# Optimization experiments

Hardware: AMD Instinct MI355X
Metric: run time of the kernel (lower is better)

## Reference

```python
import jax, jax.numpy as jnp
import numpy as np

EPS = 1e-6
LN3 = 1.0986122886681098  # ternary_softmax uses base-3 exponentials: 3**x / sum(3**x)
ROPE_BASE = 10000.0


def exact_rmsnorm(x, g):
    # ExactRMSNorm: x / sqrt(mean(x^2) + eps) * g
    ms = jnp.mean(jnp.square(x), axis=-1, keepdims=True)
    return x * jax.lax.rsqrt(ms + EPS) * g


def ternary_rope(t):
    # Rotary embedding whose cos/sin tables are quantized to {-1, 0, +1}
    # (round() of cos/sin in [-1,1] yields exactly the ternary set).
    S, D = t.shape[-2], t.shape[-1]
    half = D // 2
    inv_freq = 1.0 / (ROPE_BASE ** (jnp.arange(half, dtype=jnp.float32) / half))
    ang = jnp.arange(S, dtype=jnp.float32)[:, None] * inv_freq[None, :]  # [S, half]
    cos = jnp.round(jnp.cos(ang))
    sin = jnp.round(jnp.sin(ang))
    cos = jnp.concatenate([cos, cos], axis=-1)  # [S, D]
    sin = jnp.concatenate([sin, sin], axis=-1)
    rot = jnp.concatenate([-t[..., half:], t[..., :half]], axis=-1)
    return t * cos + rot * sin


def ternary_softmax(x, axis=-1):
    # softmax in base 3: 3**x / sum(3**x) == softmax(x * ln 3)
    return jax.nn.softmax(x * LN3, axis=axis)


def setup_inputs() -> dict:
    key = jax.random.key(0)
    ks = jax.random.split(key, 6)
    B, S, D = 4, 4096, 1024
    x = jax.random.normal(ks[0], (B, S, D), dtype=jnp.float32)
    g_norm = jnp.ones((D,), dtype=jnp.float32)
    w_qkv = jax.random.normal(ks[1], (D, 3 * D), dtype=jnp.float32) * 0.02
    b_qkv = jnp.zeros((3 * D,), dtype=jnp.float32)
    w_proj = jax.random.normal(ks[2], (D, D), dtype=jnp.float32) * 0.02
    b_proj = jnp.zeros((D,), dtype=jnp.float32)
    return {"x": x, "g_norm": g_norm, "w_qkv": w_qkv, "b_qkv": b_qkv,
            "w_proj": w_proj, "b_proj": b_proj}


def reference(x, g_norm, w_qkv, b_qkv, w_proj, b_proj):
    D = x.shape[-1]
    scale = 1.0 / jnp.sqrt(jnp.float32(D))
    residual = x
    h = exact_rmsnorm(x, g_norm)
    qkv = h @ w_qkv + b_qkv  # [B, S, 3D]
    q, k, v = jnp.split(qkv, 3, axis=-1)
    q = ternary_rope(q)
    k = ternary_rope(k)
    scores = jnp.einsum("bsd,btd->bst", q, k) * scale  # [B, S, S]
    attn = ternary_softmax(scores, axis=-1)
    o = jnp.einsum("bst,btd->bsd", attn, v)
    return o @ w_proj + b_proj + residual
```

## Files before the change

kernel.cpp:

```cpp
#include <hip/hip_runtime.h>
#include <hip/hip_fp8.h>
#include <stdint.h>

#define DEVI __device__ __forceinline__

typedef unsigned short u16;
typedef uint8_t u8;
typedef __attribute__((ext_vector_type(8))) __bf16 bf16x8;
typedef __attribute__((ext_vector_type(4))) float f32x4;
typedef __attribute__((ext_vector_type(4))) int i32x4;
typedef __attribute__((ext_vector_type(8))) int i32x8;

DEVI float b2f(u16 u) { union { unsigned int i; float f; } v; v.i = ((unsigned int)u) << 16; return v.f; }
DEVI u16 f2b(float f) {
  union { float f; unsigned int i; } v; v.f = f;
  unsigned int r = v.i + 0x7fffu + ((v.i >> 16) & 1u);
  return (u16)(r >> 16);
}
DEVI u8 f2f8(float f) { __hip_fp8_e4m3 t(f); return t.__x; }

DEVI void gld_lds16(const void* g, void* l) {
  __builtin_amdgcn_global_load_lds((const __attribute__((address_space(1))) unsigned int*)g,
                                   (__attribute__((address_space(3))) unsigned int*)l, 16, 0, 0);
}

DEVI i32x8 ld32(const u8* p0, const u8* p1) {
  i32x4 lo = *(const i32x4*)p0;
  i32x4 hi = *(const i32x4*)p1;
  return __builtin_shufflevector(lo, hi, 0, 1, 2, 3, 4, 5, 6, 7);
}


__global__ __launch_bounds__(256) void k_rmsnorm(const float* __restrict__ x,
                                                 const float* __restrict__ g,
                                                 u8* __restrict__ h) {
  const int row = blockIdx.x;
  const int t = threadIdx.x;
  const float4 v = ((const float4*)(x + (size_t)row * 1024))[t];
  float ss = v.x * v.x + v.y * v.y + v.z * v.z + v.w * v.w;
  for (int off = 32; off > 0; off >>= 1) ss += __shfl_down(ss, off);
  __shared__ float red[4];
  if ((t & 63) == 0) red[t >> 6] = ss;
  __syncthreads();
  const float tot = red[0] + red[1] + red[2] + red[3];
  const float sc = rsqrtf(tot * (1.0f / 1024.0f) + 1e-6f);
  const float4 gv = ((const float4*)g)[t];
  uchar4 o;
  o.x = f2f8(v.x * sc * gv.x); o.y = f2f8(v.y * sc * gv.y);
  o.z = f2f8(v.z * sc * gv.z); o.w = f2f8(v.w * sc * gv.w);
  *(uchar4*)(h + (size_t)row * 1024 + t * 4) = o;
}

__global__ __launch_bounds__(256) void k_transpose_cast(const float* __restrict__ src,
                                                        int rows, int cols,
                                                        u16* __restrict__ dst) {
  __shared__ float tile[32][33];
  const int c0 = blockIdx.x * 32, r0 = blockIdx.y * 32;
  const int tx = threadIdx.x, ty = threadIdx.y;
  for (int i = 0; i < 32; i += 8)
    tile[ty + i][tx] = src[(size_t)(r0 + ty + i) * cols + c0 + tx];
  __syncthreads();
  for (int i = 0; i < 32; i += 8)
    dst[(size_t)(c0 + ty + i) * rows + r0 + tx] = f2b(tile[tx][ty + i]);
}

__global__ __launch_bounds__(256) void k_transpose_cast_f8(const float* __restrict__ src,
                                                           int rows, int cols,
                                                           u8* __restrict__ dst) {
  __shared__ float tile[32][33];
  const int c0 = blockIdx.x * 32, r0 = blockIdx.y * 32;
  const int tx = threadIdx.x, ty = threadIdx.y;
  for (int i = 0; i < 32; i += 8)
    tile[ty + i][tx] = src[(size_t)(r0 + ty + i) * cols + c0 + tx];
  __syncthreads();
  for (int i = 0; i < 32; i += 8)
    dst[(size_t)(c0 + ty + i) * rows + r0 + tx] = f2f8(tile[tx][ty + i] * 32.0f);
}

__global__ __launch_bounds__(256) void k_rope_cast(const u16* __restrict__ q16, const u16* __restrict__ k16,
                                                   u8* __restrict__ q8, u8* __restrict__ k8) {
  const int row = blockIdx.x;
  const int pos = row & 4095;
  const int t = threadIdx.x;
  const int j0 = t * 2;
  float c[2], s[2];
#pragma unroll
  for (int u = 0; u < 2; u++) {
    const float e = (float)(j0 + u) * (1.0f / 512.0f);
    const float invf = exp2f(-13.287712379549449f * e);
    const float ang = (float)pos * invf;
    c[u] = rintf(cosf(ang));
    s[u] = rintf(sinf(ang));
  }
  const u16* qr = q16 + (size_t)row * 1024;
  const u16* kr = k16 + (size_t)row * 1024;
  u8* qo = q8 + (size_t)row * 1024;
  u8* ko = k8 + (size_t)row * 1024;
  const ushort2 qa = *(const ushort2*)(qr + j0), qb = *(const ushort2*)(qr + j0 + 512);
  const ushort2 ka = *(const ushort2*)(kr + j0), kb = *(const ushort2*)(kr + j0 + 512);
  uchar2 o;
  o.x = f2f8(b2f(qa.x) * c[0] - b2f(qb.x) * s[0]);
  o.y = f2f8(b2f(qa.y) * c[1] - b2f(qb.y) * s[1]);
  *(uchar2*)(qo + j0) = o;
  o.x = f2f8(b2f(qb.x) * c[0] + b2f(qa.x) * s[0]);
  o.y = f2f8(b2f(qb.y) * c[1] + b2f(qa.y) * s[1]);
  *(uchar2*)(qo + j0 + 512) = o;
  o.x = f2f8(b2f(ka.x) * c[0] - b2f(kb.x) * s[0]);
  o.y = f2f8(b2f(ka.y) * c[1] - b2f(kb.y) * s[1]);
  *(uchar2*)(ko + j0) = o;
  o.x = f2f8(b2f(kb.x) * c[0] + b2f(ka.x) * s[0]);
  o.y = f2f8(b2f(kb.y) * c[1] + b2f(ka.y) * s[1]);
  *(uchar2*)(ko + j0 + 512) = o;
}

DEVI void gemm_tile(const u16* __restrict__ A, int lda,
                    const u16* __restrict__ B, int ldb,
                    int K, int m0, int n0,
                    u16* As, u16* Bs, f32x4 acc[4][4]) {
  const int t = threadIdx.x;
  const int sr = t >> 2;
  const int sc = (t & 3) * 8;
  const u16* Ag0 = A + (size_t)(m0 + sr) * lda + sc;
  const u16* Ag1 = A + (size_t)(m0 + 64 + sr) * lda + sc;
  const u16* Bg0 = B + (size_t)(n0 + sr) * ldb + sc;
  const u16* Bg1 = B + (size_t)(n0 + 64 + sr) * ldb + sc;
  u16* Asw = As + t * 8;
  u16* Bsw = Bs + t * 8;

  const int lane = t & 63, qd = lane >> 4, l16 = lane & 15;
  const int wave = t >> 6;
  const int wm = (wave >> 1) * 64, wn = (wave & 1) * 64;
  const int aoff = (wm + l16) * 32 + qd * 8;
  const int boff = (wn + l16) * 32 + qd * 8;

  auto stage = [&](int sel, int k0) {
    u16* Ad = Asw + sel * 4096;
    u16* Bd = Bsw + sel * 4096;
    gld_lds16(Ag0 + k0, Ad);
    gld_lds16(Ag1 + k0, Ad + 2048);
    gld_lds16(Bg0 + k0, Bd);
    gld_lds16(Bg1 + k0, Bd + 2048);
  };

  stage(0, 0);
  int cur = 0;
  for (int k0 = 0; k0 < K; k0 += 32) {
    if (k0 + 32 < K) {
      stage(cur ^ 1, k0 + 32);
      asm volatile("s_waitcnt vmcnt(4)" ::: "memory");
    } else {
      asm volatile("s_waitcnt vmcnt(0)" ::: "memory");
    }
    __builtin_amdgcn_s_barrier();
    const u16* Ard = As + cur * 4096 + aoff;
    const u16* Brd = Bs + cur * 4096 + boff;
    bf16x8 af[4], bfv[4];
#pragma unroll
    for (int i = 0; i < 4; i++) af[i] = *(const bf16x8*)(Ard + i * 16 * 32);
#pragma unroll
    for (int j = 0; j < 4; j++) bfv[j] = *(const bf16x8*)(Brd + j * 16 * 32);
    __builtin_amdgcn_s_setprio(1);
#pragma unroll
    for (int i = 0; i < 4; i++)
#pragma unroll
      for (int j = 0; j < 4; j++)
        acc[i][j] = __builtin_amdgcn_mfma_f32_16x16x32_bf16(af[i], bfv[j], acc[i][j], 0, 0, 0);
    __builtin_amdgcn_s_setprio(0);
    __builtin_amdgcn_s_barrier();
    cur ^= 1;
  }
}

DEVI void gemm_tile_mx(const u8* __restrict__ A, int lda,
                       const u8* __restrict__ B, int ldb,
                       int K, int m0, int n0,
                       u8* As, u8* Bs, f32x4 acc[4][4], int sB) {
  const int t = threadIdx.x;
  const int sr = t >> 3;
  const int sc = ((t & 7) ^ (sr & 7)) << 4;
  const u8* Agb = A + (size_t)(m0 + sr) * lda + sc;
  const u8* Bgb = B + (size_t)(n0 + sr) * ldb + sc;
  u8* Asw = As + t * 16;
  u8* Bsw = Bs + t * 16;

  const int lane = t & 63, qd = lane >> 4, l16 = lane & 15;
  const int wave = t >> 6;
  const int wm = (wave >> 1) * 64, wn = (wave & 1) * 64;
  const int key = l16 & 7;
  const int c0 = ((qd << 1) ^ key) << 4;
  const int aoff = (wm + l16) * 128 + c0;
  const int boff = (wn + l16) * 128 + c0;

  auto stage = [&](int sel, int k0) {
    u8* Ad = Asw + sel * 16384;
    u8* Bd = Bsw + sel * 16384;
#pragma unroll
    for (int l = 0; l < 4; l++) {
      gld_lds16(Agb + k0 + (size_t)l * 32 * lda, Ad + l * 4096);
      gld_lds16(Bgb + k0 + (size_t)l * 32 * ldb, Bd + l * 4096);
    }
  };

  stage(0, 0);
  int cur = 0;
  for (int k0 = 0; k0 < K; k0 += 128) {
    if (k0 + 128 < K) {
      stage(cur ^ 1, k0 + 128);
      asm volatile("s_waitcnt vmcnt(8)" ::: "memory");
    } else {
      asm volatile("s_waitcnt vmcnt(0)" ::: "memory");
    }
    __builtin_amdgcn_s_barrier();
    const u8* Ab = As + cur * 16384;
    const u8* Bb = Bs + cur * 16384;
    i32x8 a[4], b[4];
#pragma unroll
    for (int i = 0; i < 4; i++)
      a[i] = ld32(Ab + aoff + i * 2048, Ab + (aoff ^ 16) + i * 2048);
#pragma unroll
    for (int j = 0; j < 4; j++)
      b[j] = ld32(Bb + boff + j * 2048, Bb + (boff ^ 16) + j * 2048);
    __builtin_amdgcn_s_setprio(1);
#pragma unroll
    for (int i = 0; i < 4; i++)
#pragma unroll
      for (int j = 0; j < 4; j++)
        acc[i][j] = __builtin_amdgcn_mfma_scale_f32_16x16x128_f8f6f4(
            a[i], b[j], acc[i][j], 0 , 0 ,
            0, 0x7f7f7f7f, 0, sB);
    __builtin_amdgcn_s_setprio(0);
    __builtin_amdgcn_s_barrier();
    cur ^= 1;
  }
}

#define ACC_INIT()                                               \
  f32x4 acc[4][4];                                               \
  _Pragma("unroll") for (int i = 0; i < 4; i++)                  \
      _Pragma("unroll") for (int j = 0; j < 4; j++)              \
          acc[i][j] = f32x4{0.f, 0.f, 0.f, 0.f};

#define GEMM_EPI_IDX()                                           \
  const int t = threadIdx.x, lane = t & 63, qd = lane >> 4,      \
            l16 = lane & 15, wave = t >> 6;                      \
  const int wm = (wave >> 1) * 64, wn = (wave & 1) * 64;         \
  (void)t;


__global__ __launch_bounds__(256) void k_gemm_qkv(const u8* __restrict__ A, const u8* __restrict__ Bt,
                                                  const float* __restrict__ bias,
                                                  u16* __restrict__ q16, u16* __restrict__ k16,
                                                  u8* __restrict__ vt) {
  __shared__ alignas(16) u8 As[32768], Bs[32768];
  ACC_INIT();
  const int m0 = blockIdx.y * 128, n0 = blockIdx.x * 128;
  gemm_tile_mx(A, 1024, Bt, 1024, 1024, m0, n0, As, Bs, acc, 0x7a7a7a7a);
  GEMM_EPI_IDX();
  const int sec = n0 >> 10;
  const int nb0 = n0 & 1023;
  if (sec < 2) {
    u16* dst = (sec == 0) ? q16 : k16;
#pragma unroll
    for (int i = 0; i < 4; i++) {
      const int mb = m0 + wm + i * 16 + qd * 4;
#pragma unroll
      for (int j = 0; j < 4; j++) {
        const int col = n0 + wn + j * 16 + l16;
        const float bv = bias[col];
        const int dcol = nb0 + wn + j * 16 + l16;
#pragma unroll
        for (int r = 0; r < 4; r++)
          dst[(size_t)(mb + r) * 1024 + dcol] = f2b(acc[i][j][r] + bv);
      }
    }
  } else {
    u8* T = As;
    const int STR = 144;
#pragma unroll
    for (int i = 0; i < 4; i++) {
      const int mloc = wm + i * 16 + qd * 4;
#pragma unroll
      for (int j = 0; j < 4; j++) {
        const int dloc = wn + j * 16 + l16;
        const float bv = bias[n0 + wn + j * 16 + l16];
#pragma unroll
        for (int r = 0; r < 4; r++)
          T[dloc * STR + mloc + r] = f2f8(acc[i][j][r] + bv);
      }
    }
    __syncthreads();
    const int b = m0 >> 12;
    const int s0 = m0 & 4095;
    const int row = t >> 1, half = (t & 1) * 64;
    u8* dst = vt + ((size_t)(b * 1024 + nb0 + row)) * 4096 + s0 + half;
#pragma unroll
    for (int c = 0; c < 4; c++)
      *(i32x4*)(dst + c * 16) = *(const i32x4*)(T + row * STR + half + c * 16);
  }
}

__global__ __launch_bounds__(256) void k_gemm_scores(const u8* __restrict__ q, const u8* __restrict__ kk,
                                                     u8* __restrict__ P, float* __restrict__ ls) {
  __shared__ alignas(16) u8 As[32768], Bs[32768];
  ACC_INIT();
  const int b = blockIdx.z;
  const u8* A = q + (size_t)b * 4096 * 1024;
  const u8* Bt = kk + (size_t)b * 4096 * 1024;
  const int bid = blockIdx.y * 32 + blockIdx.x;
  const int xcd = bid & 7, idx = bid >> 3;
  const int m0 = ((xcd >> 2) * 16 + (idx & 15)) * 128;
  const int n0 = ((xcd & 3) * 8 + (idx >> 4)) * 128;
  gemm_tile_mx(A, 1024, Bt, 1024, 1024, m0, n0, As, Bs, acc, 0x7f7f7f7f);
  GEMM_EPI_IDX();
  const float C3 = 0.04953007814753613f;
  const size_t Pb = (size_t)b * 4096 * 4096;
  f32x4 rowp[4];
#pragma unroll
  for (int i = 0; i < 4; i++) rowp[i] = f32x4{0.f, 0.f, 0.f, 0.f};
#pragma unroll
  for (int i = 0; i < 4; i++) {
    const int mb = m0 + wm + i * 16 + qd * 4;
#pragma unroll
    for (int j = 0; j < 4; j++) {
      const int col = n0 + wn + j * 16 + l16;
#pragma unroll
      for (int r = 0; r < 4; r++) {
        const float pv = __builtin_amdgcn_exp2f(acc[i][j][r] * C3);
        P[Pb + (size_t)(mb + r) * 4096 + col] = f2f8(pv);
        rowp[i][r] += pv;
      }
    }
  }
#pragma unroll
  for (int m = 1; m < 16; m <<= 1)
#pragma unroll
    for (int i = 0; i < 4; i++) {
      rowp[i].x += __shfl_xor(rowp[i].x, m);
      rowp[i].y += __shfl_xor(rowp[i].y, m);
      rowp[i].z += __shfl_xor(rowp[i].z, m);
      rowp[i].w += __shfl_xor(rowp[i].w, m);
    }
  if (l16 == 0) {
#pragma unroll
    for (int i = 0; i < 4; i++) {
      const int mb = m0 + wm + i * 16 + qd * 4;
#pragma unroll
      for (int r = 0; r < 4; r++)
        atomicAdd(ls + (size_t)b * 4096 + mb + r, rowp[i][r]);
    }
  }
}

__global__ __launch_bounds__(256) void k_gemm_pv(const u8* __restrict__ P, const u8* __restrict__ vt,
                                                 const float* __restrict__ ls, u16* __restrict__ o) {
  __shared__ alignas(16) u8 As[32768], Bs[32768];
  ACC_INIT();
  const int b = blockIdx.z;
  const u8* A = P + (size_t)b * 4096 * 4096;
  const u8* Bt = vt + (size_t)b * 1024 * 4096;
  const int bid = blockIdx.y * 8 + blockIdx.x;
  const int xcd = bid & 7, idx = bid >> 3;
  const int m0 = ((xcd >> 1) * 8 + (idx & 7)) * 128;
  const int n0 = ((xcd & 1) * 4 + (idx >> 3)) * 128;
  gemm_tile_mx(A, 4096, Bt, 4096, 4096, m0, n0, As, Bs, acc, 0x7f7f7f7f);
  GEMM_EPI_IDX();
#pragma unroll
  for (int i = 0; i < 4; i++) {
    const int mb = m0 + wm + i * 16 + qd * 4;
    f32x4 inv;
#pragma unroll
    for (int r = 0; r < 4; r++) inv[r] = 1.0f / ls[(size_t)b * 4096 + mb + r];
#pragma unroll
    for (int j = 0; j < 4; j++) {
      const int col = n0 + wn + j * 16 + l16;
#pragma unroll
      for (int r = 0; r < 4; r++)
        o[(size_t)(b * 4096 + mb + r) * 1024 + col] = f2b(acc[i][j][r] * inv[r]);
    }
  }
}

__global__ __launch_bounds__(256) void k_gemm_proj(const u16* __restrict__ A, const u16* __restrict__ Bt,
                                                   const float* __restrict__ bias, const float* __restrict__ x,
                                                   float* __restrict__ out) {
  __shared__ alignas(16) u16 As[8192], Bs[8192];
  ACC_INIT();
  const int m0 = blockIdx.y * 128, n0 = blockIdx.x * 128;
  gemm_tile(A, 1024, Bt, 1024, 1024, m0, n0, As, Bs, acc);
  GEMM_EPI_IDX();
#pragma unroll
  for (int i = 0; i < 4; i++) {
    const int mb = m0 + wm + i * 16 + qd * 4;
#pragma unroll
    for (int j = 0; j < 4; j++) {
      const int col = n0 + wn + j * 16 + l16;
      const float bv = bias[col];
#pragma unroll
      for (int r = 0; r < 4; r++) {
        const size_t idxo = (size_t)(mb + r) * 1024 + col;
        out[idxo] = acc[i][j][r] + bv + x[idxo];
      }
    }
  }
}

extern "C" void kernel_launch(void* const* d_in, const int* in_sizes, int n_in,
                              void* d_out, int out_size, void* d_ws, size_t ws_size,
                              hipStream_t stream) {
  const float* x     = (const float*)d_in[0];
  const float* g     = (const float*)d_in[1];
  const float* wqkv  = (const float*)d_in[2];
  const float* bqkv  = (const float*)d_in[3];
  const float* wproj = (const float*)d_in[4];
  const float* bproj = (const float*)d_in[5];
  float* out = (float*)d_out;

  char* wsp = (char*)d_ws;
  size_t off = 0;
  auto take = [&](size_t bytes) -> void* {
    off = (off + 255) & ~(size_t)255;
    void* r = wsp + off;
    off += bytes;
    return r;
  };
  char* hreg = (char*)take(16384ull * 1024 * 2);
  u8*  h8   = (u8*)hreg;
  u16* o16  = (u16*)hreg;
  u8*  wqT8 = (u8*)take(3072ull * 1024);
  u16* wpT  = (u16*)take(1024ull * 1024 * 2);
  u8*  q8   = (u8*)take(16384ull * 1024);
  u8*  k8   = (u8*)take(16384ull * 1024);
  u8*  vt   = (u8*)take(4ull * 1024 * 4096);
  float* ls = (float*)take(16384ull * 4);
  char* scratch = (char*)take(3ull * 16384 * 1024 * 2);
  u16* q16 = (u16*)scratch;
  u16* k16 = (u16*)(scratch + 16384ull * 1024 * 2);
  u8*  P   = (u8*)scratch;

  k_transpose_cast_f8<<<dim3(3072 / 32, 1024 / 32), dim3(32, 8), 0, stream>>>(wqkv, 1024, 3072, wqT8);
  k_transpose_cast<<<dim3(1024 / 32, 1024 / 32), dim3(32, 8), 0, stream>>>(wproj, 1024, 1024, wpT);
  k_rmsnorm<<<16384, 256, 0, stream>>>(x, g, h8);
  k_gemm_qkv<<<dim3(24, 128), 256, 0, stream>>>(h8, wqT8, bqkv, q16, k16, vt);
  k_rope_cast<<<16384, 256, 0, stream>>>(q16, k16, q8, k8);
  hipMemsetAsync(ls, 0, 16384 * 4, stream);
  k_gemm_scores<<<dim3(32, 32, 4), 256, 0, stream>>>(q8, k8, P, ls);
  k_gemm_pv<<<dim3(8, 32, 4), 256, 0, stream>>>(P, vt, ls, o16);
  k_gemm_proj<<<dim3(8, 128), 256, 0, stream>>>(o16, wpT, bproj, x, out);
}
```

Before: 456.2 us.

## Enlarge FP8 GEMM tiles to 256x256 with 8-wave blocks

Changes the FP8 MX GEMMs (QKV, scores, PV) from 128x128 tiles and 4 waves to 256x256 tiles and 8 waves, each wave covering 128x64. LDS grows to 128KB per block with double buffering, and A fragments are loaded one at a time inside the MFMA loop to hold down register use. Block-to-XCD swizzles are rewritten for the smaller grids. The aim is more operand reuse and less global/L2 traffic per FLOP. The cost is lower occupancy (one block per CU), larger accumulator register footprint, and fewer blocks for load balancing, notably 256 blocks for PV.

```diff
diff --git a/kernel.cpp b/kernel.cpp
--- a/kernel.cpp
+++ b/kernel.cpp
@@ -171,10 +171,10 @@
   }
 }
 
-DEVI void gemm_tile_mx(const u8* __restrict__ A, int lda,
-                       const u8* __restrict__ B, int ldb,
-                       int K, int m0, int n0,
-                       u8* As, u8* Bs, f32x4 acc[4][4], int sB) {
+DEVI void gemm_tile_mx2(const u8* __restrict__ A, int lda,
+                        const u8* __restrict__ B, int ldb,
+                        int K, int m0, int n0,
+                        u8* As, u8* Bs, f32x4 acc[8][4], int sB) {
   const int t = threadIdx.x;
   const int sr = t >> 3;
   const int sc = ((t & 7) ^ (sr & 7)) << 4;
@@ -185,19 +185,19 @@
 
   const int lane = t & 63, qd = lane >> 4, l16 = lane & 15;
   const int wave = t >> 6;
-  const int wm = (wave >> 1) * 64, wn = (wave & 1) * 64;
+  const int wm = (wave >> 2) * 128, wn = (wave & 3) * 64;
   const int key = l16 & 7;
   const int c0 = ((qd << 1) ^ key) << 4;
   const int aoff = (wm + l16) * 128 + c0;
   const int boff = (wn + l16) * 128 + c0;
 
   auto stage = [&](int sel, int k0) {
-    u8* Ad = Asw + sel * 16384;
-    u8* Bd = Bsw + sel * 16384;
+    u8* Ad = Asw + sel * 32768;
+    u8* Bd = Bsw + sel * 32768;
 #pragma unroll
     for (int l = 0; l < 4; l++) {
-      gld_lds16(Agb + k0 + (size_t)l * 32 * lda, Ad + l * 4096);
-      gld_lds16(Bgb + k0 + (size_t)l * 32 * ldb, Bd + l * 4096);
+      gld_lds16(Agb + k0 + (size_t)l * 64 * lda, Ad + l * 8192);
+      gld_lds16(Bgb + k0 + (size_t)l * 64 * ldb, Bd + l * 8192);
     }
   };
 
@@ -211,57 +211,70 @@
       asm volatile("s_waitcnt vmcnt(0)" ::: "memory");
     }
     __builtin_amdgcn_s_barrier();
-    const u8* Ab = As + cur * 16384;
-    const u8* Bb = Bs + cur * 16384;
-    i32x8 a[4], b[4];
-#pragma unroll
-    for (int i = 0; i < 4; i++)
-      a[i] = ld32(Ab + aoff + i * 2048, Ab + (aoff ^ 16) + i * 2048);
+    const u8* Ab = As + cur * 32768;
+    const u8* Bb = Bs + cur * 32768;
+    i32x8 b[4];
 #pragma unroll
     for (int j = 0; j < 4; j++)
       b[j] = ld32(Bb + boff + j * 2048, Bb + (boff ^ 16) + j * 2048);
-    __builtin_amdgcn_s_setprio(1);
-#pragma unroll
-    for (int i = 0; i < 4; i++)
+#pragma unroll
+    for (int i = 0; i < 8; i++) {
+      const i32x8 a = ld32(Ab + aoff + i * 2048, Ab + (aoff ^ 16) + i * 2048);
+      __builtin_amdgcn_s_setprio(1);
 #pragma unroll
       for (int j = 0; j < 4; j++)
         acc[i][j] = __builtin_amdgcn_mfma_scale_f32_16x16x128_f8f6f4(
-            a[i], b[j], acc[i][j], 0 , 0 ,
+            a, b[j], acc[i][j], 0 , 0 ,
             0, 0x7f7f7f7f, 0, sB);
-    __builtin_amdgcn_s_setprio(0);
+      __builtin_amdgcn_s_setprio(0);
+    }
     __builtin_amdgcn_s_barrier();
     cur ^= 1;
   }
 }
 
-#define ACC_INIT()                                               \
+#define ACC_INIT4()                                              \
   f32x4 acc[4][4];                                               \
   _Pragma("unroll") for (int i = 0; i < 4; i++)                  \
       _Pragma("unroll") for (int j = 0; j < 4; j++)              \
           acc[i][j] = f32x4{0.f, 0.f, 0.f, 0.f};
 
-#define GEMM_EPI_IDX()                                           \
+#define ACC_INIT8()                                              \
+  f32x4 acc[8][4];                                               \
+  _Pragma("unroll") for (int i = 0; i < 8; i++)                  \
+      _Pragma("unroll") for (int j = 0; j < 4; j++)              \
+          acc[i][j] = f32x4{0.f, 0.f, 0.f, 0.f};
+
+#define GEMM_EPI_IDX4()                                          \
   const int t = threadIdx.x, lane = t & 63, qd = lane >> 4,      \
             l16 = lane & 15, wave = t >> 6;                      \
   const int wm = (wave >> 1) * 64, wn = (wave & 1) * 64;         \
   (void)t;
 
-
-__global__ __launch_bounds__(256) void k_gemm_qkv(const u8* __restrict__ A, const u8* __restrict__ Bt,
+#define GEMM_EPI_IDX8()                                          \
+  const int t = threadIdx.x, lane = t & 63, qd = lane >> 4,      \
+            l16 = lane & 15, wave = t >> 6;                      \
+  const int wm = (wave >> 2) * 128, wn = (wave & 3) * 64;        \
+  (void)t;
+
+
+__global__ __launch_bounds__(512) void k_gemm_qkv(const u8* __restrict__ A, const u8* __restrict__ Bt,
                                                   const float* __restrict__ bias,
                                                   u16* __restrict__ q16, u16* __restrict__ k16,
                                                   u8* __restrict__ vt) {
-  __shared__ alignas(16) u8 As[32768], Bs[32768];
-  ACC_INIT();
-  const int m0 = blockIdx.y * 128, n0 = blockIdx.x * 128;
-  gemm_tile_mx(A, 1024, Bt, 1024, 1024, m0, n0, As, Bs, acc, 0x7a7a7a7a);
-  GEMM_EPI_IDX();
+  __shared__ alignas(16) u8 SMEM[131072];
+  u8* As = SMEM;
+  u8* Bs = SMEM + 65536;
+  ACC_INIT8();
+  const int m0 = blockIdx.y * 256, n0 = blockIdx.x * 256;
+  gemm_tile_mx2(A, 1024, Bt, 1024, 1024, m0, n0, As, Bs, acc, 0x7a7a7a7a);
+  GEMM_EPI_IDX8();
   const int sec = n0 >> 10;
   const int nb0 = n0 & 1023;
   if (sec < 2) {
     u16* dst = (sec == 0) ? q16 : k16;
 #pragma unroll
-    for (int i = 0; i < 4; i++) {
+    for (int i = 0; i < 8; i++) {
       const int mb = m0 + wm + i * 16 + qd * 4;
 #pragma unroll
       for (int j = 0; j < 4; j++) {
@@ -274,10 +287,10 @@
       }
     }
   } else {
-    u8* T = As;
-    const int STR = 144;
-#pragma unroll
-    for (int i = 0; i < 4; i++) {
+    u8* T = SMEM;
+    const int STR = 272;
+#pragma unroll
+    for (int i = 0; i < 8; i++) {
       const int mloc = wm + i * 16 + qd * 4;
 #pragma unroll
       for (int j = 0; j < 4; j++) {
@@ -291,34 +304,37 @@
     __syncthreads();
     const int b = m0 >> 12;
     const int s0 = m0 & 4095;
-    const int row = t >> 1, half = (t & 1) * 64;
+    const int row = t >> 1, half = (t & 1) * 128;
     u8* dst = vt + ((size_t)(b * 1024 + nb0 + row)) * 4096 + s0 + half;
-#pragma unroll
-    for (int c = 0; c < 4; c++)
-      *(i32x4*)(dst + c * 16) = *(const i32x4*)(T + row * STR + half + c * 16);
-  }
-}
-
-__global__ __launch_bounds__(256) void k_gemm_scores(const u8* __restrict__ q, const u8* __restrict__ kk,
+    const u8* src = T + row * STR + half;
+#pragma unroll
+    for (int c = 0; c < 8; c++)
+      *(i32x4*)(dst + c * 16) = *(const i32x4*)(src + c * 16);
+  }
+}
+
+__global__ __launch_bounds__(512) void k_gemm_scores(const u8* __restrict__ q, const u8* __restrict__ kk,
                                                      u8* __restrict__ P, float* __restrict__ ls) {
-  __shared__ alignas(16) u8 As[32768], Bs[32768];
-  ACC_INIT();
+  __shared__ alignas(16) u8 SMEM[131072];
+  u8* As = SMEM;
+  u8* Bs = SMEM + 65536;
+  ACC_INIT8();
   const int b = blockIdx.z;
   const u8* A = q + (size_t)b * 4096 * 1024;
   const u8* Bt = kk + (size_t)b * 4096 * 1024;
-  const int bid = blockIdx.y * 32 + blockIdx.x;
+  const int bid = blockIdx.y * 16 + blockIdx.x;
   const int xcd = bid & 7, idx = bid >> 3;
-  const int m0 = ((xcd >> 2) * 16 + (idx & 15)) * 128;
-  const int n0 = ((xcd & 3) * 8 + (idx >> 4)) * 128;
-  gemm_tile_mx(A, 1024, Bt, 1024, 1024, m0, n0, As, Bs, acc, 0x7f7f7f7f);
-  GEMM_EPI_IDX();
+  const int m0 = (idx & 15) * 256;
+  const int n0 = ((xcd << 1) | (idx >> 4)) * 256;
+  gemm_tile_mx2(A, 1024, Bt, 1024, 1024, m0, n0, As, Bs, acc, 0x7f7f7f7f);
+  GEMM_EPI_IDX8();
   const float C3 = 0.04953007814753613f;
   const size_t Pb = (size_t)b * 4096 * 4096;
-  f32x4 rowp[4];
-#pragma unroll
-  for (int i = 0; i < 4; i++) rowp[i] = f32x4{0.f, 0.f, 0.f, 0.f};
-#pragma unroll
-  for (int i = 0; i < 4; i++) {
+  f32x4 rowp[8];
+#pragma unroll
+  for (int i = 0; i < 8; i++) rowp[i] = f32x4{0.f, 0.f, 0.f, 0.f};
+#pragma unroll
+  for (int i = 0; i < 8; i++) {
     const int mb = m0 + wm + i * 16 + qd * 4;
 #pragma unroll
     for (int j = 0; j < 4; j++) {
@@ -334,7 +350,7 @@
 #pragma unroll
   for (int m = 1; m < 16; m <<= 1)
 #pragma unroll
-    for (int i = 0; i < 4; i++) {
+    for (int i = 0; i < 8; i++) {
       rowp[i].x += __shfl_xor(rowp[i].x, m);
       rowp[i].y += __shfl_xor(rowp[i].y, m);
       rowp[i].z += __shfl_xor(rowp[i].z, m);
@@ -342,7 +358,7 @@
     }
   if (l16 == 0) {
 #pragma unroll
-    for (int i = 0; i < 4; i++) {
+    for (int i = 0; i < 8; i++) {
       const int mb = m0 + wm + i * 16 + qd * 4;
 #pragma unroll
       for (int r = 0; r < 4; r++)
@@ -351,21 +367,23 @@
   }
 }
 
-__global__ __launch_bounds__(256) void k_gemm_pv(const u8* __restrict__ P, const u8* __restrict__ vt,
+__global__ __launch_bounds__(512) void k_gemm_pv(const u8* __restrict__ P, const u8* __restrict__ vt,
                                                  const float* __restrict__ ls, u16* __restrict__ o) {
-  __shared__ alignas(16) u8 As[32768], Bs[32768];
-  ACC_INIT();
+  __shared__ alignas(16) u8 SMEM[131072];
+  u8* As = SMEM;
+  u8* Bs = SMEM + 65536;
+  ACC_INIT8();
   const int b = blockIdx.z;
   const u8* A = P + (size_t)b * 4096 * 4096;
   const u8* Bt = vt + (size_t)b * 1024 * 4096;
-  const int bid = blockIdx.y * 8 + blockIdx.x;
+  const int bid = blockIdx.y * 4 + blockIdx.x;
   const int xcd = bid & 7, idx = bid >> 3;
-  const int m0 = ((xcd >> 1) * 8 + (idx & 7)) * 128;
-  const int n0 = ((xcd & 1) * 4 + (idx >> 3)) * 128;
-  gemm_tile_mx(A, 4096, Bt, 4096, 4096, m0, n0, As, Bs, acc, 0x7f7f7f7f);
-  GEMM_EPI_IDX();
-#pragma unroll
-  for (int i = 0; i < 4; i++) {
+  const int m0 = (((xcd & 1) << 3) | idx) * 256;
+  const int n0 = (xcd >> 1) * 256;
+  gemm_tile_mx2(A, 4096, Bt, 4096, 4096, m0, n0, As, Bs, acc, 0x7f7f7f7f);
+  GEMM_EPI_IDX8();
+#pragma unroll
+  for (int i = 0; i < 8; i++) {
     const int mb = m0 + wm + i * 16 + qd * 4;
     f32x4 inv;
 #pragma unroll
@@ -384,10 +402,10 @@
                                                    const float* __restrict__ bias, const float* __restrict__ x,
                                                    float* __restrict__ out) {
   __shared__ alignas(16) u16 As[8192], Bs[8192];
-  ACC_INIT();
+  ACC_INIT4();
   const int m0 = blockIdx.y * 128, n0 = blockIdx.x * 128;
   gemm_tile(A, 1024, Bt, 1024, 1024, m0, n0, As, Bs, acc);
-  GEMM_EPI_IDX();
+  GEMM_EPI_IDX4();
 #pragma unroll
   for (int i = 0; i < 4; i++) {
     const int mb = m0 + wm + i * 16 + qd * 4;
@@ -440,10 +458,10 @@
   k_transpose_cast_f8<<<dim3(3072 / 32, 1024 / 32), dim3(32, 8), 0, stream>>>(wqkv, 1024, 3072, wqT8);
   k_transpose_cast<<<dim3(1024 / 32, 1024 / 32), dim3(32, 8), 0, stream>>>(wproj, 1024, 1024, wpT);
   k_rmsnorm<<<16384, 256, 0, stream>>>(x, g, h8);
-  k_gemm_qkv<<<dim3(24, 128), 256, 0, stream>>>(h8, wqT8, bqkv, q16, k16, vt);
+  k_gemm_qkv<<<dim3(12, 64), 512, 0, stream>>>(h8, wqT8, bqkv, q16, k16, vt);
   k_rope_cast<<<16384, 256, 0, stream>>>(q16, k16, q8, k8);
   hipMemsetAsync(ls, 0, 16384 * 4, stream);
-  k_gemm_scores<<<dim3(32, 32, 4), 256, 0, stream>>>(q8, k8, P, ls);
-  k_gemm_pv<<<dim3(8, 32, 4), 256, 0, stream>>>(P, vt, ls, o16);
+  k_gemm_scores<<<dim3(16, 16, 4), 512, 0, stream>>>(q8, k8, P, ls);
+  k_gemm_pv<<<dim3(4, 16, 4), 512, 0, stream>>>(P, vt, ls, o16);
   k_gemm_proj<<<dim3(8, 128), 256, 0, stream>>>(o16, wpT, bproj, x, out);
 }
```

After: 465.9 us. +2.1%, slower.
